# Kernel optimization log

Measured on AMD Instinct MI355X. Metric: run time of the kernel, lower is better.

## Reference

```python
import jax, jax.numpy as jnp
import numpy as np

B, T, D, H = 64, 1024, 256, 128
NTAG = 3

def setup_inputs():
    key = jax.random.key(0)
    ks = jax.random.split(key, 24)
    sc = 1.0 / float(np.sqrt(H))
    def u(k, shape):
        return jax.random.uniform(k, shape, jnp.float32, -sc, sc)
    inp = {'x': jax.random.normal(ks[0], (B, T, D), jnp.float32),
           'tags': jax.random.randint(ks[1], (B, T), 0, NTAG)}
    i = 2
    for name, din in (('l0', D), ('l0r', D), ('l1', 2 * H), ('l1r', 2 * H)):
        kk = jax.random.split(ks[i], 4); i += 1
        inp['w_ih_' + name] = u(kk[0], (4 * H, din))
        inp['w_hh_' + name] = u(kk[1], (4 * H, H))
        inp['b_ih_' + name] = u(kk[2], (4 * H,))
        inp['b_hh_' + name] = u(kk[3], (4 * H,))
    inp['fc_w'] = u(ks[i], (NTAG, 2 * H)); i += 1
    inp['fc_b'] = u(ks[i], (NTAG,)); i += 1
    inp['crf_start'] = 0.1 * jax.random.normal(ks[i], (NTAG,), jnp.float32); i += 1
    inp['crf_end'] = 0.1 * jax.random.normal(ks[i], (NTAG,), jnp.float32); i += 1
    inp['crf_trans'] = 0.1 * jax.random.normal(ks[i], (NTAG, NTAG), jnp.float32)
    return inp

def _lstm_dir(x, w_ih, w_hh, b_ih, b_hh, reverse):
    # x: [B,T,Din] -> h: [B,T,H]; torch gate order: i, f, g, o
    gx = jnp.einsum('btd,gd->btg', x, w_ih) + b_ih + b_hh  # [B,T,4H]
    gx = jnp.swapaxes(gx, 0, 1)                            # [T,B,4H]
    h0 = jnp.zeros((x.shape[0], H), x.dtype)
    def step(carry, g):
        h, c = carry
        g = g + h @ w_hh.T
        i_, f_, g_, o_ = jnp.split(g, 4, axis=-1)
        c = jax.nn.sigmoid(f_) * c + jax.nn.sigmoid(i_) * jnp.tanh(g_)
        h = jax.nn.sigmoid(o_) * jnp.tanh(c)
        return (h, c), h
    _, hs = jax.lax.scan(step, (h0, h0), gx, reverse=reverse)
    return jnp.swapaxes(hs, 0, 1)

def _bilstm(x, p):
    out = x
    for name in ('l0', 'l1'):
        f = _lstm_dir(out, p['w_ih_' + name], p['w_hh_' + name], p['b_ih_' + name], p['b_hh_' + name], False)
        b = _lstm_dir(out, p['w_ih_' + name + 'r'], p['w_hh_' + name + 'r'], p['b_ih_' + name + 'r'], p['b_hh_' + name + 'r'], True)
        out = jnp.concatenate([f, b], axis=-1)  # [B,T,2H]
    return out

def _crf_nll(emissions, tags, start, end, trans):
    # numerator: score of the gold tag path
    em_sc = jnp.take_along_axis(emissions, tags[..., None], axis=2)[..., 0].sum(axis=1)
    num = start[tags[:, 0]] + em_sc + trans[tags[:, :-1], tags[:, 1:]].sum(axis=1) + end[tags[:, -1]]
    # denominator: forward algorithm (log-domain DP scan over time)
    alpha0 = start[None, :] + emissions[:, 0]     # [B,NTAG]
    ems = jnp.swapaxes(emissions[:, 1:], 0, 1)    # [T-1,B,NTAG]
    def step(alpha, em_t):
        alpha = jax.nn.logsumexp(alpha[:, :, None] + trans[None] + em_t[:, None, :], axis=1)
        return alpha, None
    alpha, _ = jax.lax.scan(step, alpha0, ems)
    logZ = jax.nn.logsumexp(alpha + end[None, :], axis=1)
    return -jnp.mean(num - logZ)  # reduction='mean', negated

def reference(x, tags, w_ih_l0, w_hh_l0, b_ih_l0, b_hh_l0, w_ih_l0r, w_hh_l0r, b_ih_l0r, b_hh_l0r, w_ih_l1, w_hh_l1, b_ih_l1, b_hh_l1, w_ih_l1r, w_hh_l1r, b_ih_l1r, b_hh_l1r, fc_w, fc_b, crf_start, crf_end, crf_trans):
    p = dict(w_ih_l0=w_ih_l0, w_hh_l0=w_hh_l0, b_ih_l0=b_ih_l0, b_hh_l0=b_hh_l0,
             w_ih_l0r=w_ih_l0r, w_hh_l0r=w_hh_l0r, b_ih_l0r=b_ih_l0r, b_hh_l0r=b_hh_l0r,
             w_ih_l1=w_ih_l1, w_hh_l1=w_hh_l1, b_ih_l1=b_ih_l1, b_hh_l1=b_hh_l1,
             w_ih_l1r=w_ih_l1r, w_hh_l1r=w_hh_l1r, b_ih_l1r=b_ih_l1r, b_hh_l1r=b_hh_l1r)
    out = _bilstm(x, p)                      # [B,T,2H]
    emissions = out @ fc_w.T + fc_b          # dropout is identity in eval mode
    loss = _crf_nll(emissions, tags, crf_start, crf_end, crf_trans)
    return (loss, emissions)
```

## Files before the change

### kernel.cpp

```cpp
#include <hip/hip_runtime.h>
#include <cstdint>

#define BB 64
#define TT 1024
#define DD 256
#define HH 128
#define G4 512
#define NTAG 3

typedef __attribute__((ext_vector_type(8))) short bf16x8;
typedef __attribute__((ext_vector_type(4))) float f32x4;
typedef __attribute__((ext_vector_type(4))) int i32x4;

__device__ __forceinline__ unsigned short f2bf(float f) {
    uint32_t u = __builtin_bit_cast(uint32_t, f);
    uint32_t r = (u + 0x7FFFu + ((u >> 16) & 1u)) >> 16;
    return (unsigned short)r;
}
__device__ __forceinline__ float bf2f(unsigned short s) {
    uint32_t u = ((uint32_t)s) << 16;
    return __builtin_bit_cast(float, u);
}
__device__ __forceinline__ float sigm(float x) {
    return __builtin_amdgcn_rcpf(1.f + __builtin_amdgcn_exp2f(x * -1.44269504f));
}
__device__ __forceinline__ float tanh_f(float x) {
    return 1.f - 2.f * __builtin_amdgcn_rcpf(1.f + __builtin_amdgcn_exp2f(x * 2.88539008f));
}

__device__ __forceinline__ void block_sync_lds() {
    __builtin_amdgcn_s_waitcnt(0xC07F);
    __builtin_amdgcn_s_barrier();
}

#define ASYNC16(gp, lp) \
    __builtin_amdgcn_global_load_lds((const __attribute__((address_space(1))) unsigned int*)(gp), \
                                     (__attribute__((address_space(3))) unsigned int*)(lp), 16, 0, 0)

__global__ void cvt4_kernel(const float* __restrict__ in, unsigned short* __restrict__ out, int n4) {
    int idx = blockIdx.x * blockDim.x + threadIdx.x;
    if (idx < n4) {
        float4 v = ((const float4*)in)[idx];
        ushort4 o;
        o.x = f2bf(v.x); o.y = f2bf(v.y); o.z = f2bf(v.z); o.w = f2bf(v.w);
        ((ushort4*)out)[idx] = o;
    }
}

__global__ __launch_bounds__(256) void gemm_ih(
    const unsigned short* __restrict__ A,
    const unsigned short* __restrict__ W0, const unsigned short* __restrict__ W1,
    const float* __restrict__ bih0, const float* __restrict__ bhh0,
    const float* __restrict__ bih1, const float* __restrict__ bhh1,
    unsigned short* __restrict__ G0, unsigned short* __restrict__ G1)
{
    const int dir = blockIdx.z;
    const unsigned short* W = dir ? W1 : W0;
    const float* bih = dir ? bih1 : bih0;
    const float* bhh = dir ? bhh1 : bhh0;
    unsigned short* G = dir ? G1 : G0;

    const int gate = blockIdx.y;
    const int m0 = blockIdx.x * 128;

    const int tid = threadIdx.x;
    const int wv = tid >> 6;
    const int lane = tid & 63;
    const int m16 = lane & 15;
    const int quad = lane >> 4;
    const int wave_m = wv & 1;
    const int wave_n = wv >> 1;

    __shared__ __align__(16) unsigned short As[128 * 64];
    __shared__ __align__(16) unsigned short Bs[128 * 64];

    f32x4 acc[4][4];
#pragma unroll
    for (int i = 0; i < 4; i++)
#pragma unroll
        for (int j = 0; j < 4; j++) acc[i][j] = (f32x4){0.f, 0.f, 0.f, 0.f};

    const int lrow = lane >> 3;
    const int lcol = (lane & 7) * 8;

    for (int kt = 0; kt < 4; kt++) {
#pragma unroll
        for (int it = 0; it < 4; it++) {
            const int seg = wv * 4 + it;
            const int row = seg * 8 + lrow;
            ASYNC16(A + (size_t)(m0 + row) * DD + kt * 64 + lcol, As + seg * 512);
            ASYNC16(W + (size_t)(gate * 128 + row) * DD + kt * 64 + lcol, Bs + seg * 512);
        }
        __syncthreads();

#pragma unroll
        for (int kk = 0; kk < 2; kk++) {
            bf16x8 a[4], b[4];
#pragma unroll
            for (int i = 0; i < 4; i++) {
                const int row = wave_m * 64 + i * 16 + m16;
                a[i] = __builtin_bit_cast(bf16x8, *(const uint4*)&As[row * 64 + kk * 32 + quad * 8]);
            }
#pragma unroll
            for (int j = 0; j < 4; j++) {
                const int row = wave_n * 64 + j * 16 + m16;
                b[j] = __builtin_bit_cast(bf16x8, *(const uint4*)&Bs[row * 64 + kk * 32 + quad * 8]);
            }
#pragma unroll
            for (int i = 0; i < 4; i++)
#pragma unroll
                for (int j = 0; j < 4; j++)
                    acc[i][j] = __builtin_amdgcn_mfma_f32_16x16x32_bf16(a[i], b[j], acc[i][j], 0, 0, 0);
        }
        __syncthreads();
    }

#pragma unroll
    for (int j = 0; j < 4; j++) {
        const int hcol = wave_n * 64 + j * 16 + m16;
        const int n = gate * 128 + hcol;
        const float bias = bih[n] + bhh[n];
        const int col = hcol * 4 + gate;
#pragma unroll
        for (int i = 0; i < 4; i++) {
            const int rowg = m0 + wave_m * 64 + i * 16 + quad * 4;
#pragma unroll
            for (int r = 0; r < 4; r++) {
                G[(size_t)(rowg + r) * G4 + col] = f2bf(acc[i][j][r] + bias);
            }
        }
    }
}

__global__ __launch_bounds__(512, 2) void lstm_scan_mfma(
    const unsigned short* __restrict__ Gf, const unsigned short* __restrict__ Gr,
    const float* __restrict__ whh_f, const float* __restrict__ whh_r,
    unsigned short* __restrict__ out)
{
    const int b = blockIdx.x;
    const int dir = blockIdx.y;
    const unsigned short* G = dir ? Gr : Gf;
    const float* W = dir ? whh_r : whh_f;

    const int tid = threadIdx.x;
    const int wv = tid >> 6;
    const int lane = tid & 63;
    const int n16 = lane & 15;
    const int quad = lane >> 4;

    __shared__ __align__(16) signed char h8[2][HH];

    i32x4 bfrag[4][2];
#pragma unroll
    for (int p = 0; p < 4; p++) {
        const int n = 128 * p + wv * 16 + n16;
        const float* Wr = W + (size_t)n * HH;
#pragma unroll
        for (int kc = 0; kc < 2; kc++) {
            union { signed char c[16]; i32x4 v; } u;
#pragma unroll
            for (int j = 0; j < 16; j++) {
                float w = Wr[kc * 64 + quad * 16 + j] * 1024.f;
                int q = (int)rintf(w);
                q = q > 127 ? 127 : (q < -127 ? -127 : q);
                u.c[j] = (signed char)q;
            }
            bfrag[p][kc] = u.v;
        }
    }

    if (tid < HH) h8[0][tid] = 0;

    const bool dense = (quad == 0);
    const int hcol = wv * 16 + n16;
    float c = 0.f;
    const float INV = 1.f / 130048.f;

    const unsigned short* gb = G + (size_t)b * TT * G4 + hcol * 4;

    ushort4 gq[4];
#pragma unroll
    for (int d = 0; d < 4; d++) {
        const int t = dir ? (TT - 1 - d) : d;
        gq[d] = *(const ushort4*)(gb + (size_t)t * G4);
    }
    block_sync_lds();

    for (int sb = 0; sb < TT; sb += 4) {
#pragma unroll
        for (int d = 0; d < 4; d++) {
            const int s = sb + d;
            const int t = dir ? (TT - 1 - s) : s;
            const int buf = s & 1;

            i32x4 af[2];
#pragma unroll
            for (int kc = 0; kc < 2; kc++)
                af[kc] = __builtin_bit_cast(i32x4, *(const uint4*)&h8[buf][kc * 64 + quad * 16]);

            i32x4 acc[4];
#pragma unroll
            for (int p = 0; p < 4; p++) {
                i32x4 a = {0, 0, 0, 0};
                a = __builtin_amdgcn_mfma_i32_16x16x64_i8(af[0], bfrag[p][0], a, 0, 0, 0);
                a = __builtin_amdgcn_mfma_i32_16x16x64_i8(af[1], bfrag[p][1], a, 0, 0, 0);
                acc[p] = a;
            }

            if (dense) {
                const float gi = (float)acc[0][0] * INV + bf2f(gq[d].x);
                const float gf = (float)acc[1][0] * INV + bf2f(gq[d].y);
                const float gg = (float)acc[2][0] * INV + bf2f(gq[d].z);
                const float go = (float)acc[3][0] * INV + bf2f(gq[d].w);
                const float ig = sigm(gi);
                const float fg = sigm(gf);
                const float gt = tanh_f(gg);
                const float og = sigm(go);
                c = fg * c + ig * gt;
                const float h = og * tanh_f(c);
                h8[buf ^ 1][hcol] = (signed char)(int)rintf(h * 127.f);
                out[((size_t)b * TT + t) * (2 * HH) + dir * HH + hcol] = f2bf(h);
            }

            {
                int sn = s + 4;
                int tn = dir ? (TT - 1 - sn) : sn;
                tn = tn < 0 ? 0 : (tn > TT - 1 ? TT - 1 : tn);
                gq[d] = *(const ushort4*)(gb + (size_t)tn * G4);
            }
            block_sync_lds();
        }
    }
}

__global__ __launch_bounds__(256) void emis_kernel(
    const unsigned short* __restrict__ out1,
    const float* __restrict__ fcw, const float* __restrict__ fcb,
    float* __restrict__ dout)
{
    if (blockIdx.x == 0 && threadIdx.x == 0) dout[0] = 0.f;

    __shared__ float wsm[NTAG * 256];
    for (int i = threadIdx.x; i < NTAG * 256; i += 256) wsm[i] = fcw[i];
    __syncthreads();

    const int bt = blockIdx.x * 256 + threadIdx.x;
    float a0 = fcb[0], a1 = fcb[1], a2 = fcb[2];
    const uint4* row = (const uint4*)(out1 + (size_t)bt * 256);
#pragma unroll 4
    for (int k8 = 0; k8 < 32; k8++) {
        uint4 u = row[k8];
        const int kb = k8 * 8;
        uint32_t p[4] = {u.x, u.y, u.z, u.w};
#pragma unroll
        for (int e = 0; e < 4; e++) {
            float flo = __builtin_bit_cast(float, p[e] << 16);
            float fhi = __builtin_bit_cast(float, p[e] & 0xFFFF0000u);
            const int k = kb + 2 * e;
            a0 = fmaf(flo, wsm[0 * 256 + k], a0);
            a1 = fmaf(flo, wsm[1 * 256 + k], a1);
            a2 = fmaf(flo, wsm[2 * 256 + k], a2);
            a0 = fmaf(fhi, wsm[0 * 256 + k + 1], a0);
            a1 = fmaf(fhi, wsm[1 * 256 + k + 1], a1);
            a2 = fmaf(fhi, wsm[2 * 256 + k + 1], a2);
        }
    }
    dout[1 + (size_t)bt * 3 + 0] = a0;
    dout[1 + (size_t)bt * 3 + 1] = a1;
    dout[1 + (size_t)bt * 3 + 2] = a2;
}

__device__ __forceinline__ float sel3(int i, float a, float b, float c) {
    return i == 0 ? a : (i == 1 ? b : c);
}
__device__ __forceinline__ float lse3(float a, float b, float c) {
    float m = fmaxf(a, fmaxf(b, c));
    float s = exp2f((a - m) * 1.44269504f) + exp2f((b - m) * 1.44269504f) + exp2f((c - m) * 1.44269504f);
    return m + log2f(s) * 0.69314718f;
}

__global__ __launch_bounds__(64) void crf_kernel(
    const int* __restrict__ tags,
    const float* __restrict__ start, const float* __restrict__ end,
    const float* __restrict__ trans, float* __restrict__ dout)
{
    const int b = blockIdx.x;
    const int th = threadIdx.x;
    const float* em = dout + 1 + (size_t)b * TT * 3;
    const int* tg = tags + (size_t)b * TT;

    float tr[3][3];
#pragma unroll
    for (int i = 0; i < 3; i++)
#pragma unroll
        for (int j = 0; j < 3; j++) tr[i][j] = trans[i * 3 + j];

    float P[3][3];
#pragma unroll
    for (int i = 0; i < 3; i++)
#pragma unroll
        for (int j = 0; j < 3; j++) P[i][j] = (i == j) ? 0.f : -1e30f;

    const int t0 = 1 + 16 * th;
    float numpart = 0.f;
    int tprev = tg[t0 - 1];

    for (int d = 0; d < 16; d++) {
        const int t = t0 + d;
        if (t < TT) {
            const float e0 = em[3 * t + 0], e1 = em[3 * t + 1], e2 = em[3 * t + 2];
            float N[3][3];
#pragma unroll
            for (int i = 0; i < 3; i++) {
                N[i][0] = lse3(P[i][0] + tr[0][0], P[i][1] + tr[1][0], P[i][2] + tr[2][0]) + e0;
                N[i][1] = lse3(P[i][0] + tr[0][1], P[i][1] + tr[1][1], P[i][2] + tr[2][1]) + e1;
                N[i][2] = lse3(P[i][0] + tr[0][2], P[i][1] + tr[1][2], P[i][2] + tr[2][2]) + e2;
            }
#pragma unroll
            for (int i = 0; i < 3; i++)
#pragma unroll
                for (int j = 0; j < 3; j++) P[i][j] = N[i][j];
            const int tc = tg[t];
            numpart += sel3(tc, e0, e1, e2) + sel3(tprev,
                         sel3(tc, tr[0][0], tr[0][1], tr[0][2]),
                         sel3(tc, tr[1][0], tr[1][1], tr[1][2]),
                         sel3(tc, tr[2][0], tr[2][1], tr[2][2]));
            tprev = tc;
        }
    }

#pragma unroll
    for (int off = 1; off < 64; off <<= 1) {
        float Q[3][3];
#pragma unroll
        for (int i = 0; i < 3; i++)
#pragma unroll
            for (int j = 0; j < 3; j++) Q[i][j] = __shfl_xor(P[i][j], off, 64);
        const bool hi = (th & off) != 0;
        float L[3][3], R[3][3];
#pragma unroll
        for (int i = 0; i < 3; i++)
#pragma unroll
            for (int j = 0; j < 3; j++) {
                L[i][j] = hi ? Q[i][j] : P[i][j];
                R[i][j] = hi ? P[i][j] : Q[i][j];
            }
#pragma unroll
        for (int i = 0; i < 3; i++)
#pragma unroll
            for (int j = 0; j < 3; j++)
                P[i][j] = lse3(L[i][0] + R[0][j], L[i][1] + R[1][j], L[i][2] + R[2][j]);
        numpart += __shfl_xor(numpart, off, 64);
    }

    if (th == 0) {
        const int tg0 = tg[0], tgL = tg[TT - 1];
        const float a0 = start[0] + em[0], a1 = start[1] + em[1], a2 = start[2] + em[2];
        const float f0 = lse3(a0 + P[0][0], a1 + P[1][0], a2 + P[2][0]);
        const float f1 = lse3(a0 + P[0][1], a1 + P[1][1], a2 + P[2][1]);
        const float f2 = lse3(a0 + P[0][2], a1 + P[1][2], a2 + P[2][2]);
        const float logZ = lse3(f0 + end[0], f1 + end[1], f2 + end[2]);
        const float num = sel3(tg0, start[0], start[1], start[2]) +
                          sel3(tg0, em[0], em[1], em[2]) + numpart +
                          sel3(tgL, end[0], end[1], end[2]);
        atomicAdd(&dout[0], (logZ - num) * (1.0f / (float)BB));
    }
}

extern "C" void kernel_launch(void* const* d_in, const int* in_sizes, int n_in,
                              void* d_out, int out_size, void* d_ws, size_t ws_size,
                              hipStream_t stream) {
    const float* x        = (const float*)d_in[0];
    const int*   tags     = (const int*)d_in[1];
    const float* w_ih_l0  = (const float*)d_in[2];
    const float* w_hh_l0  = (const float*)d_in[3];
    const float* b_ih_l0  = (const float*)d_in[4];
    const float* b_hh_l0  = (const float*)d_in[5];
    const float* w_ih_l0r = (const float*)d_in[6];
    const float* w_hh_l0r = (const float*)d_in[7];
    const float* b_ih_l0r = (const float*)d_in[8];
    const float* b_hh_l0r = (const float*)d_in[9];
    const float* w_ih_l1  = (const float*)d_in[10];
    const float* w_hh_l1  = (const float*)d_in[11];
    const float* b_ih_l1  = (const float*)d_in[12];
    const float* b_hh_l1  = (const float*)d_in[13];
    const float* w_ih_l1r = (const float*)d_in[14];
    const float* w_hh_l1r = (const float*)d_in[15];
    const float* b_ih_l1r = (const float*)d_in[16];
    const float* b_hh_l1r = (const float*)d_in[17];
    const float* fc_w     = (const float*)d_in[18];
    const float* fc_b     = (const float*)d_in[19];
    const float* crf_start= (const float*)d_in[20];
    const float* crf_end  = (const float*)d_in[21];
    const float* crf_trans= (const float*)d_in[22];
    float* dout = (float*)d_out;

    uint8_t* ws = (uint8_t*)d_ws;
    unsigned short* xb   = (unsigned short*)(ws + 0);
    unsigned short* out1 = xb;
    unsigned short* out0 = (unsigned short*)(ws + 33554432);
    unsigned short* Gf   = (unsigned short*)(ws + 67108864);
    unsigned short* Gr   = (unsigned short*)(ws + 134217728);
    unsigned short* wb0  = (unsigned short*)(ws + 201326592);
    unsigned short* wb0r = wb0 + 131072;
    unsigned short* wb1  = wb0 + 262144;
    unsigned short* wb1r = wb0 + 393216;

    cvt4_kernel<<<dim3((16777216 / 4 + 255) / 256), dim3(256), 0, stream>>>(x, xb, 16777216 / 4);
    cvt4_kernel<<<dim3(128), dim3(256), 0, stream>>>(w_ih_l0,  wb0,  131072 / 4);
    cvt4_kernel<<<dim3(128), dim3(256), 0, stream>>>(w_ih_l0r, wb0r, 131072 / 4);
    cvt4_kernel<<<dim3(128), dim3(256), 0, stream>>>(w_ih_l1,  wb1,  131072 / 4);
    cvt4_kernel<<<dim3(128), dim3(256), 0, stream>>>(w_ih_l1r, wb1r, 131072 / 4);

    gemm_ih<<<dim3(512, 4, 2), dim3(256), 0, stream>>>(
        xb, wb0, wb0r, b_ih_l0, b_hh_l0, b_ih_l0r, b_hh_l0r, Gf, Gr);
    lstm_scan_mfma<<<dim3(64, 2), dim3(512), 0, stream>>>(Gf, Gr, w_hh_l0, w_hh_l0r, out0);

    gemm_ih<<<dim3(512, 4, 2), dim3(256), 0, stream>>>(
        out0, wb1, wb1r, b_ih_l1, b_hh_l1, b_ih_l1r, b_hh_l1r, Gf, Gr);
    lstm_scan_mfma<<<dim3(64, 2), dim3(512), 0, stream>>>(Gf, Gr, w_hh_l1, w_hh_l1r, out1);

    emis_kernel<<<dim3(256), dim3(256), 0, stream>>>(out1, fc_w, fc_b, dout);

    crf_kernel<<<dim3(64), dim3(64), 0, stream>>>(tags, crf_start, crf_end, crf_trans, dout);
}
```

Measured before the change: 1.168 ms.

## Store input-gate preactivations as per-gate planes with vectorized GEMM epilogue

The input-projection GEMM swaps its MFMA operand order so each lane holds four consecutive hidden columns. It then writes bf16 gate values into four separate gate planes of [B*T,128] with 8-byte vector stores, replacing the strided scalar stores into an interleaved [.,512] layout. The recurrent scan now reads the four gates with four scalar 2-byte loads from the separate planes instead of one 8-byte load. The aim is cheaper, coalesced epilogue stores in the GEMM, at the cost of more and scattered loads inside the latency-bound scan loop.

```diff
diff --git a/kernel.cpp b/kernel.cpp
--- a/kernel.cpp
+++ b/kernel.cpp
@@ -7,6 +7,7 @@
 #define HH 128
 #define G4 512
 #define NTAG 3
+#define PS 8388608
 
 typedef __attribute__((ext_vector_type(8))) short bf16x8;
 typedef __attribute__((ext_vector_type(4))) float f32x4;
@@ -110,24 +111,32 @@
             for (int i = 0; i < 4; i++)
 #pragma unroll
                 for (int j = 0; j < 4; j++)
-                    acc[i][j] = __builtin_amdgcn_mfma_f32_16x16x32_bf16(a[i], b[j], acc[i][j], 0, 0, 0);
+                    acc[i][j] = __builtin_amdgcn_mfma_f32_16x16x32_bf16(b[j], a[i], acc[i][j], 0, 0, 0);
         }
         __syncthreads();
     }
 
-#pragma unroll
-    for (int j = 0; j < 4; j++) {
-        const int hcol = wave_n * 64 + j * 16 + m16;
-        const int n = gate * 128 + hcol;
-        const float bias = bih[n] + bhh[n];
-        const int col = hcol * 4 + gate;
-#pragma unroll
-        for (int i = 0; i < 4; i++) {
-            const int rowg = m0 + wave_m * 64 + i * 16 + quad * 4;
-#pragma unroll
-            for (int r = 0; r < 4; r++) {
-                G[(size_t)(rowg + r) * G4 + col] = f2bf(acc[i][j][r] + bias);
-            }
+    unsigned short* Gp = G + (size_t)gate * PS;
+    float bias[4][4];
+#pragma unroll
+    for (int j = 0; j < 4; j++)
+#pragma unroll
+        for (int r = 0; r < 4; r++) {
+            const int n = gate * 128 + wave_n * 64 + j * 16 + quad * 4 + r;
+            bias[j][r] = bih[n] + bhh[n];
+        }
+#pragma unroll
+    for (int i = 0; i < 4; i++) {
+        const int row = m0 + wave_m * 64 + i * 16 + m16;
+#pragma unroll
+        for (int j = 0; j < 4; j++) {
+            const int colbase = wave_n * 64 + j * 16 + quad * 4;
+            ushort4 v;
+            v.x = f2bf(acc[i][j][0] + bias[j][0]);
+            v.y = f2bf(acc[i][j][1] + bias[j][1]);
+            v.z = f2bf(acc[i][j][2] + bias[j][2]);
+            v.w = f2bf(acc[i][j][3] + bias[j][3]);
+            *(ushort4*)(Gp + (size_t)row * 128 + colbase) = v;
         }
     }
 }
@@ -176,13 +185,17 @@
     float c = 0.f;
     const float INV = 1.f / 130048.f;
 
-    const unsigned short* gb = G + (size_t)b * TT * G4 + hcol * 4;
+    const unsigned short* gbL = G + (size_t)b * TT * 128 + hcol;
 
     ushort4 gq[4];
 #pragma unroll
     for (int d = 0; d < 4; d++) {
         const int t = dir ? (TT - 1 - d) : d;
-        gq[d] = *(const ushort4*)(gb + (size_t)t * G4);
+        const unsigned short* gp = gbL + (size_t)t * 128;
+        gq[d].x = gp[0];
+        gq[d].y = gp[PS];
+        gq[d].z = gp[2 * PS];
+        gq[d].w = gp[3 * PS];
     }
     block_sync_lds();
 
@@ -226,7 +239,11 @@
                 int sn = s + 4;
                 int tn = dir ? (TT - 1 - sn) : sn;
                 tn = tn < 0 ? 0 : (tn > TT - 1 ? TT - 1 : tn);
-                gq[d] = *(const ushort4*)(gb + (size_t)tn * G4);
+                const unsigned short* gp = gbL + (size_t)tn * 128;
+                gq[d].x = gp[0];
+                gq[d].y = gp[PS];
+                gq[d].z = gp[2 * PS];
+                gq[d].w = gp[3 * PS];
             }
             block_sync_lds();
         }
```

Measured after the change: 1.138 ms. -2.6%, faster.

## Pre-permute input weights for vectorized gate stores and halve scan block size

Applied to the files above, without the earlier changes.

Input-projection weights are converted to bf16 with rows reordered so that each hidden unit's four gates sit next to each other. The GEMM swaps its MFMA operands, so each lane writes four adjacent gate columns as one ushort4 instead of scattered 2-byte stores. The recurrent scan now runs with 256 threads: each wave covers two 16-column hidden groups and lanes in quads 0 and 1 both do useful gate math, which cuts the waves taking part in each per-step barrier. The cost is twice the MFMA work and weight registers per wave, which may reduce occupancy.

```diff
diff --git a/kernel.cpp b/kernel.cpp
--- a/kernel.cpp
+++ b/kernel.cpp
@@ -45,6 +45,17 @@
         o.x = f2bf(v.x); o.y = f2bf(v.y); o.z = f2bf(v.z); o.w = f2bf(v.w);
         ((ushort4*)out)[idx] = o;
     }
+}
+
+__global__ void cvtperm_kernel(const float* __restrict__ in, unsigned short* __restrict__ out) {
+    const int idx = blockIdx.x * 256 + threadIdx.x;
+    const int np = idx >> 6;
+    const int k4 = idx & 63;
+    const int g = np & 3, h = np >> 2;
+    float4 v = ((const float4*)(in + (size_t)(g * 128 + h) * DD))[k4];
+    ushort4 o;
+    o.x = f2bf(v.x); o.y = f2bf(v.y); o.z = f2bf(v.z); o.w = f2bf(v.w);
+    ((ushort4*)(out + (size_t)np * DD))[k4] = o;
 }
 
 __global__ __launch_bounds__(256) void gemm_ih(
@@ -60,7 +71,7 @@
     const float* bhh = dir ? bhh1 : bhh0;
     unsigned short* G = dir ? G1 : G0;
 
-    const int gate = blockIdx.y;
+    const int nstrip = blockIdx.y;
     const int m0 = blockIdx.x * 128;
 
     const int tid = threadIdx.x;
@@ -89,7 +100,7 @@
             const int seg = wv * 4 + it;
             const int row = seg * 8 + lrow;
             ASYNC16(A + (size_t)(m0 + row) * DD + kt * 64 + lcol, As + seg * 512);
-            ASYNC16(W + (size_t)(gate * 128 + row) * DD + kt * 64 + lcol, Bs + seg * 512);
+            ASYNC16(W + (size_t)(nstrip * 128 + row) * DD + kt * 64 + lcol, Bs + seg * 512);
         }
         __syncthreads();
 
@@ -110,29 +121,37 @@
             for (int i = 0; i < 4; i++)
 #pragma unroll
                 for (int j = 0; j < 4; j++)
-                    acc[i][j] = __builtin_amdgcn_mfma_f32_16x16x32_bf16(a[i], b[j], acc[i][j], 0, 0, 0);
+                    acc[i][j] = __builtin_amdgcn_mfma_f32_16x16x32_bf16(b[j], a[i], acc[i][j], 0, 0, 0);
         }
         __syncthreads();
     }
 
-#pragma unroll
-    for (int j = 0; j < 4; j++) {
-        const int hcol = wave_n * 64 + j * 16 + m16;
-        const int n = gate * 128 + hcol;
-        const float bias = bih[n] + bhh[n];
-        const int col = hcol * 4 + gate;
-#pragma unroll
-        for (int i = 0; i < 4; i++) {
-            const int rowg = m0 + wave_m * 64 + i * 16 + quad * 4;
-#pragma unroll
-            for (int r = 0; r < 4; r++) {
-                G[(size_t)(rowg + r) * G4 + col] = f2bf(acc[i][j][r] + bias);
-            }
-        }
-    }
-}
-
-__global__ __launch_bounds__(512, 2) void lstm_scan_mfma(
+    float bias[4][4];
+#pragma unroll
+    for (int j = 0; j < 4; j++)
+#pragma unroll
+        for (int r = 0; r < 4; r++) {
+            const int np = nstrip * 128 + wave_n * 64 + j * 16 + quad * 4 + r;
+            const int g = np & 3, h = np >> 2;
+            bias[j][r] = bih[g * 128 + h] + bhh[g * 128 + h];
+        }
+#pragma unroll
+    for (int i = 0; i < 4; i++) {
+        const int row = m0 + wave_m * 64 + i * 16 + m16;
+#pragma unroll
+        for (int j = 0; j < 4; j++) {
+            const int colbase = nstrip * 128 + wave_n * 64 + j * 16 + quad * 4;
+            ushort4 v;
+            v.x = f2bf(acc[i][j][0] + bias[j][0]);
+            v.y = f2bf(acc[i][j][1] + bias[j][1]);
+            v.z = f2bf(acc[i][j][2] + bias[j][2]);
+            v.w = f2bf(acc[i][j][3] + bias[j][3]);
+            *(ushort4*)(G + (size_t)row * G4 + colbase) = v;
+        }
+    }
+}
+
+__global__ __launch_bounds__(256) void lstm_scan_mfma(
     const unsigned short* __restrict__ Gf, const unsigned short* __restrict__ Gr,
     const float* __restrict__ whh_f, const float* __restrict__ whh_r,
     unsigned short* __restrict__ out)
@@ -147,32 +166,34 @@
     const int lane = tid & 63;
     const int n16 = lane & 15;
     const int quad = lane >> 4;
+    const int q = quad & 1;
 
     __shared__ __align__(16) signed char h8[2][HH];
 
-    i32x4 bfrag[4][2];
-#pragma unroll
-    for (int p = 0; p < 4; p++) {
-        const int n = 128 * p + wv * 16 + n16;
-        const float* Wr = W + (size_t)n * HH;
-#pragma unroll
-        for (int kc = 0; kc < 2; kc++) {
-            union { signed char c[16]; i32x4 v; } u;
-#pragma unroll
-            for (int j = 0; j < 16; j++) {
-                float w = Wr[kc * 64 + quad * 16 + j] * 1024.f;
-                int q = (int)rintf(w);
-                q = q > 127 ? 127 : (q < -127 ? -127 : q);
-                u.c[j] = (signed char)q;
-            }
-            bfrag[p][kc] = u.v;
-        }
-    }
+    i32x4 bfrag[4][2][2];
+#pragma unroll
+    for (int g = 0; g < 4; g++)
+#pragma unroll
+        for (int u = 0; u < 2; u++) {
+            const int n = g * 128 + (2 * wv + u) * 16 + n16;
+            const float* Wr = W + (size_t)n * HH;
+#pragma unroll
+            for (int kc = 0; kc < 2; kc++) {
+                union { signed char c[16]; i32x4 v; } uu;
+#pragma unroll
+                for (int j = 0; j < 16; j++) {
+                    float w = Wr[kc * 64 + quad * 16 + j] * 1024.f;
+                    int qq = (int)rintf(w);
+                    qq = qq > 127 ? 127 : (qq < -127 ? -127 : qq);
+                    uu.c[j] = (signed char)qq;
+                }
+                bfrag[g][u][kc] = uu.v;
+            }
+        }
 
     if (tid < HH) h8[0][tid] = 0;
 
-    const bool dense = (quad == 0);
-    const int hcol = wv * 16 + n16;
+    const int hcol = (2 * wv + q) * 16 + n16;
     float c = 0.f;
     const float INV = 1.f / 130048.f;
 
@@ -198,26 +219,28 @@
             for (int kc = 0; kc < 2; kc++)
                 af[kc] = __builtin_bit_cast(i32x4, *(const uint4*)&h8[buf][kc * 64 + quad * 16]);
 
-            i32x4 acc[4];
-#pragma unroll
-            for (int p = 0; p < 4; p++) {
-                i32x4 a = {0, 0, 0, 0};
-                a = __builtin_amdgcn_mfma_i32_16x16x64_i8(af[0], bfrag[p][0], a, 0, 0, 0);
-                a = __builtin_amdgcn_mfma_i32_16x16x64_i8(af[1], bfrag[p][1], a, 0, 0, 0);
-                acc[p] = a;
-            }
-
-            if (dense) {
-                const float gi = (float)acc[0][0] * INV + bf2f(gq[d].x);
-                const float gf = (float)acc[1][0] * INV + bf2f(gq[d].y);
-                const float gg = (float)acc[2][0] * INV + bf2f(gq[d].z);
-                const float go = (float)acc[3][0] * INV + bf2f(gq[d].w);
-                const float ig = sigm(gi);
-                const float fg = sigm(gf);
-                const float gt = tanh_f(gg);
-                const float og = sigm(go);
-                c = fg * c + ig * gt;
-                const float h = og * tanh_f(c);
+            i32x4 acc[4][2];
+#pragma unroll
+            for (int g = 0; g < 4; g++)
+#pragma unroll
+                for (int u = 0; u < 2; u++) {
+                    i32x4 a = {0, 0, 0, 0};
+                    a = __builtin_amdgcn_mfma_i32_16x16x64_i8(af[0], bfrag[g][u][0], a, 0, 0, 0);
+                    a = __builtin_amdgcn_mfma_i32_16x16x64_i8(af[1], bfrag[g][u][1], a, 0, 0, 0);
+                    acc[g][u] = a;
+                }
+
+            const float gi = (float)acc[0][q][0] * INV + bf2f(gq[d].x);
+            const float gf = (float)acc[1][q][0] * INV + bf2f(gq[d].y);
+            const float gg = (float)acc[2][q][0] * INV + bf2f(gq[d].z);
+            const float go = (float)acc[3][q][0] * INV + bf2f(gq[d].w);
+            const float ig = sigm(gi);
+            const float fg = sigm(gf);
+            const float gt = tanh_f(gg);
+            const float og = sigm(go);
+            c = fg * c + ig * gt;
+            const float h = og * tanh_f(c);
+            if (quad < 2) {
                 h8[buf ^ 1][hcol] = (signed char)(int)rintf(h * 127.f);
                 out[((size_t)b * TT + t) * (2 * HH) + dir * HH + hcol] = f2bf(h);
             }
@@ -407,18 +430,18 @@
     unsigned short* wb1r = wb0 + 393216;
 
     cvt4_kernel<<<dim3((16777216 / 4 + 255) / 256), dim3(256), 0, stream>>>(x, xb, 16777216 / 4);
-    cvt4_kernel<<<dim3(128), dim3(256), 0, stream>>>(w_ih_l0,  wb0,  131072 / 4);
-    cvt4_kernel<<<dim3(128), dim3(256), 0, stream>>>(w_ih_l0r, wb0r, 131072 / 4);
-    cvt4_kernel<<<dim3(128), dim3(256), 0, stream>>>(w_ih_l1,  wb1,  131072 / 4);
-    cvt4_kernel<<<dim3(128), dim3(256), 0, stream>>>(w_ih_l1r, wb1r, 131072 / 4);
+    cvtperm_kernel<<<dim3(128), dim3(256), 0, stream>>>(w_ih_l0,  wb0);
+    cvtperm_kernel<<<dim3(128), dim3(256), 0, stream>>>(w_ih_l0r, wb0r);
+    cvtperm_kernel<<<dim3(128), dim3(256), 0, stream>>>(w_ih_l1,  wb1);
+    cvtperm_kernel<<<dim3(128), dim3(256), 0, stream>>>(w_ih_l1r, wb1r);
 
     gemm_ih<<<dim3(512, 4, 2), dim3(256), 0, stream>>>(
         xb, wb0, wb0r, b_ih_l0, b_hh_l0, b_ih_l0r, b_hh_l0r, Gf, Gr);
-    lstm_scan_mfma<<<dim3(64, 2), dim3(512), 0, stream>>>(Gf, Gr, w_hh_l0, w_hh_l0r, out0);
+    lstm_scan_mfma<<<dim3(64, 2), dim3(256), 0, stream>>>(Gf, Gr, w_hh_l0, w_hh_l0r, out0);
 
     gemm_ih<<<dim3(512, 4, 2), dim3(256), 0, stream>>>(
         out0, wb1, wb1r, b_ih_l1, b_hh_l1, b_ih_l1r, b_hh_l1r, Gf, Gr);
-    lstm_scan_mfma<<<dim3(64, 2), dim3(512), 0, stream>>>(Gf, Gr, w_hh_l1, w_hh_l1r, out1);
+    lstm_scan_mfma<<<dim3(64, 2), dim3(256), 0, stream>>>(Gf, Gr, w_hh_l1, w_hh_l1r, out1);
 
     emis_kernel<<<dim3(256), dim3(256), 0, stream>>>(out1, fc_w, fc_b, dout);
 
```

Result: slower. 2.818 ms (+141.2%).
